# Performance work log

Measured on AMD Instinct MI355X. Metric: run time of the kernel, lower is better.

The kernel has to match this reference:

```python
import jax, jax.numpy as jnp
import numpy as np

N_NODES = 100000


def gcn_conv(x, edge_index, W, b, num_nodes):
    """PyG GCNConv: add self-loops, symmetric deg^{-1/2} normalization,
    aggregate (x @ W) over edges, then add bias."""
    loop = jnp.arange(num_nodes, dtype=edge_index.dtype)
    src = jnp.concatenate([edge_index[0], loop])  # [E+N]
    dst = jnp.concatenate([edge_index[1], loop])
    deg = jax.ops.segment_sum(jnp.ones_like(dst, dtype=x.dtype), dst,
                              num_segments=num_nodes)  # in-degree incl. self-loop
    dinv = jnp.where(deg > 0, jax.lax.rsqrt(deg), 0.0)
    norm = dinv[src] * dinv[dst]  # [E+N]
    h = x @ W  # [N, F_out] -- transform BEFORE gather (small F_out)
    msg = h[src] * norm[:, None]  # [E+N, F_out]
    out = jax.ops.segment_sum(msg, dst, num_segments=num_nodes)
    return out + b


def setup_inputs() -> dict:
    key = jax.random.key(0)
    k1, k2, k3, k4 = jax.random.split(key, 4)
    N, E, F_in, F_hid, F_out = N_NODES, 3200000, 128, 16, 64
    x = jax.random.normal(k1, (N, F_in), dtype=jnp.float32)
    edge_index = jax.random.randint(k2, (2, E), 0, N, dtype=jnp.int64)
    # glorot-ish init for weights, zeros bias (PyG default: glorot W, zeros b)
    W1 = jax.random.normal(k3, (F_in, F_hid), dtype=jnp.float32) * (1.0 / np.sqrt(F_in))
    b1 = jnp.zeros((F_hid,), dtype=jnp.float32)
    W2 = jax.random.normal(k4, (F_hid, F_out), dtype=jnp.float32) * (1.0 / np.sqrt(F_hid))
    b2 = jnp.zeros((F_out,), dtype=jnp.float32)
    return {"x": x, "edge_index": edge_index, "W1": W1, "b1": b1, "W2": W2, "b2": b2}


def reference(x, edge_index, W1, b1, W2, b2):
    N = x.shape[0]
    h = gcn_conv(x, edge_index, W1, b1, N)
    h = jax.nn.relu(h)
    # F.dropout with training=False (inference) is identity
    h = gcn_conv(h, edge_index, W2, b2, N)
    return jax.nn.log_softmax(h, axis=1)
```

## Files before the change

kernel.cpp:

```cpp
#include <hip/hip_runtime.h>

#define FIN 128
#define FH  16
#define FO  64
#define GB  128
#define MAXNB 1024
#define CHUNK 16384

__device__ __forceinline__ unsigned pack_bf16x2(float a, float b) {
    unsigned ua = __float_as_uint(a), ub = __float_as_uint(b);
    ua = (ua + 0x7fffu + ((ua >> 16) & 1u)) >> 16;
    ub = (ub + 0x7fffu + ((ub >> 16) & 1u)) >> 16;
    return ua | (ub << 16);
}

__device__ __forceinline__ float2 unpack_bf16x2(unsigned u) {
    float2 r;
    r.x = __uint_as_float(u << 16);
    r.y = __uint_as_float(u & 0xffff0000u);
    return r;
}

__global__ __launch_bounds__(1024) void k_bscatter(const int* __restrict__ src,
                                                   const int* __restrict__ dst,
                                                   int* __restrict__ bfill,
                                                   int* __restrict__ bedge,
                                                   int E, int slab) {
    __shared__ int h[MAXNB];
    __shared__ int scanp[1024];
    __shared__ int stage[CHUNK];
    int t = threadIdx.x;
    int c0 = blockIdx.x * CHUNK;
    int c1 = min(c0 + CHUNK, E);

    h[t] = 0;
    __syncthreads();
    const int4* dst4 = (const int4*)dst;
    const int4* src4 = (const int4*)src;
    int i4b = c0 >> 2;
    int i4e = (c0 + ((c1 - c0) & ~3)) >> 2;
    for (int i = i4b + t; i < i4e; i += 1024) {
        int4 d = dst4[i];
        atomicAdd(&h[d.x >> 7], 1);
        atomicAdd(&h[d.y >> 7], 1);
        atomicAdd(&h[d.z >> 7], 1);
        atomicAdd(&h[d.w >> 7], 1);
    }
    for (int e = (i4e << 2) + t; e < c1; e += 1024)
        atomicAdd(&h[dst[e] >> 7], 1);
    __syncthreads();

    int a = h[t];
    scanp[t] = a;
    __syncthreads();
    for (int off = 1; off < 1024; off <<= 1) {
        int u = (t >= off) ? scanp[t - off] : 0;
        __syncthreads();
        scanp[t] += u;
        __syncthreads();
    }
    int lo = scanp[t] - a;

    int r = 0;
    if (a) r = atomicAdd(&bfill[t], a);
    int navail = slab - r; if (navail < 0) navail = 0;
    int hi = lo + min(a, navail);
    h[t] = lo;
    __syncthreads();

    for (int i = i4b + t; i < i4e; i += 1024) {
        int4 d = dst4[i];
        int4 s = src4[i];
        int p;
        p = atomicAdd(&h[d.x >> 7], 1); stage[p] = ((d.x & 127) << 17) | s.x;
        p = atomicAdd(&h[d.y >> 7], 1); stage[p] = ((d.y & 127) << 17) | s.y;
        p = atomicAdd(&h[d.z >> 7], 1); stage[p] = ((d.z & 127) << 17) | s.z;
        p = atomicAdd(&h[d.w >> 7], 1); stage[p] = ((d.w & 127) << 17) | s.w;
    }
    for (int e = (i4e << 2) + t; e < c1; e += 1024) {
        int d = dst[e];
        int p = atomicAdd(&h[d >> 7], 1);
        stage[p] = ((d & 127) << 17) | src[e];
    }
    __syncthreads();

    int db = t * slab + r - lo;
    int p = lo;
    for (; p < hi && ((db + p) & 3); ++p) bedge[db + p] = stage[p];
    for (; p + 3 < hi; p += 4) {
        int4 v;
        v.x = stage[p]; v.y = stage[p + 1]; v.z = stage[p + 2]; v.w = stage[p + 3];
        *(int4*)(bedge + db + p) = v;
    }
    for (; p < hi; ++p) bedge[db + p] = stage[p];
}

__global__ __launch_bounds__(256) void k_nsg(const int* __restrict__ bfill,
                                             const int* __restrict__ bedge,
                                             const float* __restrict__ x,
                                             const float* __restrict__ W1,
                                             int* __restrict__ sorted_src,
                                             int* __restrict__ counts,
                                             int* __restrict__ row_start,
                                             float* __restrict__ dinv,
                                             uint2* __restrict__ hs1u2,
                                             int N, int slab) {
    __shared__ int hist[GB];
    __shared__ int fill[GB];
    __shared__ float dinvL[GB];
    __shared__ float4 w4[FIN * FH / 4];
    int t = threadIdx.x, b = blockIdx.x;
    int base = b << 7;
    int nn = min(GB, N - base);
    if (nn <= 0) return;

    int ebeg = b * slab;
    int eend = ebeg + min(bfill[b], slab);
    if (t < GB) hist[t] = 0;
    __syncthreads();
    for (int e = ebeg + t; e < eend; e += 256)
        atomicAdd(&hist[bedge[e] >> 17], 1);
    __syncthreads();
    int c = (t < GB) ? hist[t] : 0;
    for (int off = 1; off < GB; off <<= 1) {
        int u = (t < GB && t >= off) ? hist[t - off] : 0;
        __syncthreads();
        if (t < GB) hist[t] += u;
        __syncthreads();
    }
    int excl = (t < GB) ? hist[t] - c : 0;
    if (t < nn) {
        counts[base + t] = c;
        row_start[base + t] = ebeg + excl;
        float dv = rsqrtf((float)(c + 1));
        dinv[base + t] = dv;
        dinvL[t] = dv;
        fill[t] = ebeg + excl;
    }
    __syncthreads();
    for (int e = ebeg + t; e < eend; e += 256) {
        int v = bedge[e];
        int p = atomicAdd(&fill[v >> 17], 1);
        sorted_src[p] = v & 0x1FFFF;
    }
    for (int i = t; i < FIN * FH / 4; i += 256) w4[i] = ((const float4*)W1)[i];
    __syncthreads();

    int fg = t & 3, rg = t >> 2;
    int r0l = rg * 2;
    if (r0l >= nn) return;
    int r1l = min(r0l + 1, nn - 1);
    int r0 = base + r0l, r1 = base + r1l;
    const float4* xa4 = (const float4*)(x + (long long)r0 * FIN);
    const float4* xb4 = (const float4*)(x + (long long)r1 * FIN);
    float4 a0 = make_float4(0.f, 0.f, 0.f, 0.f);
    float4 a1 = make_float4(0.f, 0.f, 0.f, 0.f);
#pragma unroll 2
    for (int k4 = 0; k4 < FIN / 4; ++k4) {
        float4 xa = xa4[k4];
        float4 xb = xb4[k4];
        const float4* wp = &w4[k4 * 16 + fg];
        float4 w0 = wp[0], w1 = wp[4], w2 = wp[8], w3 = wp[12];
        a0.x = fmaf(xa.x, w0.x, a0.x); a0.y = fmaf(xa.x, w0.y, a0.y);
        a0.z = fmaf(xa.x, w0.z, a0.z); a0.w = fmaf(xa.x, w0.w, a0.w);
        a0.x = fmaf(xa.y, w1.x, a0.x); a0.y = fmaf(xa.y, w1.y, a0.y);
        a0.z = fmaf(xa.y, w1.z, a0.z); a0.w = fmaf(xa.y, w1.w, a0.w);
        a0.x = fmaf(xa.z, w2.x, a0.x); a0.y = fmaf(xa.z, w2.y, a0.y);
        a0.z = fmaf(xa.z, w2.z, a0.z); a0.w = fmaf(xa.z, w2.w, a0.w);
        a0.x = fmaf(xa.w, w3.x, a0.x); a0.y = fmaf(xa.w, w3.y, a0.y);
        a0.z = fmaf(xa.w, w3.z, a0.z); a0.w = fmaf(xa.w, w3.w, a0.w);
        a1.x = fmaf(xb.x, w0.x, a1.x); a1.y = fmaf(xb.x, w0.y, a1.y);
        a1.z = fmaf(xb.x, w0.z, a1.z); a1.w = fmaf(xb.x, w0.w, a1.w);
        a1.x = fmaf(xb.y, w1.x, a1.x); a1.y = fmaf(xb.y, w1.y, a1.y);
        a1.z = fmaf(xb.y, w1.z, a1.z); a1.w = fmaf(xb.y, w1.w, a1.w);
        a1.x = fmaf(xb.z, w2.x, a1.x); a1.y = fmaf(xb.z, w2.y, a1.y);
        a1.z = fmaf(xb.z, w2.z, a1.z); a1.w = fmaf(xb.z, w2.w, a1.w);
        a1.x = fmaf(xb.w, w3.x, a1.x); a1.y = fmaf(xb.w, w3.y, a1.y);
        a1.z = fmaf(xb.w, w3.z, a1.z); a1.w = fmaf(xb.w, w3.w, a1.w);
    }
    float d0 = dinvL[r0l];
    uint2 o0;
    o0.x = pack_bf16x2(a0.x * d0, a0.y * d0);
    o0.y = pack_bf16x2(a0.z * d0, a0.w * d0);
    hs1u2[r0 * 4 + fg] = o0;
    if (r1l != r0l) {
        float d1 = dinvL[r1l];
        uint2 o1;
        o1.x = pack_bf16x2(a1.x * d1, a1.y * d1);
        o1.y = pack_bf16x2(a1.z * d1, a1.w * d1);
        hs1u2[r1 * 4 + fg] = o1;
    }
}

__global__ __launch_bounds__(256) void k_gather1(const int* __restrict__ rs,
                                                 const int* __restrict__ cnt,
                                                 const int* __restrict__ ss,
                                                 const unsigned* __restrict__ hs1u,
                                                 const float* __restrict__ dinv,
                                                 const float* __restrict__ b1,
                                                 unsigned* __restrict__ h1su, int n) {
    int t = threadIdx.x;
    int lane = t & 63;
    int l32 = lane & 31, g4 = l32 >> 3, f2 = l32 & 7;
    int node = blockIdx.x * 8 + ((t >> 6) << 1) + (lane >> 5);
    bool act = (node < n);
    int beg = 0, end = 0;
    unsigned uself = 0;
    float di = 0.0f;
    if (act) {
        beg = rs[node]; end = beg + cnt[node];
        uself = hs1u[node * 8 + f2];
        di = dinv[node];
    }
    float ax = 0.0f, ay = 0.0f;
    int e = beg + g4;
    for (; e + 28 < end; e += 32) {
        int s0 = ss[e],      s1 = ss[e + 4],  s2 = ss[e + 8],  s3 = ss[e + 12];
        int s4 = ss[e + 16], s5 = ss[e + 20], s6 = ss[e + 24], s7 = ss[e + 28];
        unsigned u0 = hs1u[s0 * 8 + f2], u1 = hs1u[s1 * 8 + f2];
        unsigned u2 = hs1u[s2 * 8 + f2], u3 = hs1u[s3 * 8 + f2];
        unsigned u4 = hs1u[s4 * 8 + f2], u5 = hs1u[s5 * 8 + f2];
        unsigned u6 = hs1u[s6 * 8 + f2], u7 = hs1u[s7 * 8 + f2];
        float2 p0 = unpack_bf16x2(u0), p1 = unpack_bf16x2(u1);
        float2 p2 = unpack_bf16x2(u2), p3 = unpack_bf16x2(u3);
        float2 p4 = unpack_bf16x2(u4), p5 = unpack_bf16x2(u5);
        float2 p6 = unpack_bf16x2(u6), p7 = unpack_bf16x2(u7);
        ax += ((p0.x + p1.x) + (p2.x + p3.x)) + ((p4.x + p5.x) + (p6.x + p7.x));
        ay += ((p0.y + p1.y) + (p2.y + p3.y)) + ((p4.y + p5.y) + (p6.y + p7.y));
    }
    for (; e + 4 < end; e += 8) {
        int s0 = ss[e], s1 = ss[e + 4];
        unsigned u0 = hs1u[s0 * 8 + f2], u1 = hs1u[s1 * 8 + f2];
        float2 p0 = unpack_bf16x2(u0), p1 = unpack_bf16x2(u1);
        ax += p0.x + p1.x; ay += p0.y + p1.y;
    }
    if (e < end) {
        float2 p = unpack_bf16x2(hs1u[ss[e] * 8 + f2]);
        ax += p.x; ay += p.y;
    }
    ax += __shfl_xor(ax, 8, 64);  ay += __shfl_xor(ay, 8, 64);
    ax += __shfl_xor(ax, 16, 64); ay += __shfl_xor(ay, 16, 64);
    if (act) {
        float2 s = unpack_bf16x2(uself);
        ax += s.x; ay += s.y;
        float2 bb = ((const float2*)b1)[f2];
        float v0 = fmaxf(fmaf(di, ax, bb.x), 0.0f) * di;
        float v1 = fmaxf(fmaf(di, ay, bb.y), 0.0f) * di;
        if (l32 < 8) h1su[node * 8 + f2] = pack_bf16x2(v0, v1);
    }
}

__global__ __launch_bounds__(256) void k_agg2f(const int* __restrict__ rs,
                                               const int* __restrict__ cnt,
                                               const int* __restrict__ ss,
                                               const unsigned* __restrict__ h1su,
                                               const float* __restrict__ dinv,
                                               const float* __restrict__ W2,
                                               const float* __restrict__ b2,
                                               float* __restrict__ out, int n) {
    int t = threadIdx.x;
    int lane = t & 63, g8 = lane >> 3, f2 = lane & 7;
    int node = blockIdx.x * 4 + (t >> 6);
    if (node >= n) return;
    float w[FH];
#pragma unroll
    for (int j = 0; j < FH; ++j) w[j] = W2[j * FO + lane];
    int beg = rs[node], end = beg + cnt[node];
    float ax = 0.0f, ay = 0.0f;
    int e = beg + g8;
    for (; e + 8 < end; e += 16) {
        unsigned u0 = h1su[ss[e] * 8 + f2];
        unsigned u1 = h1su[ss[e + 8] * 8 + f2];
        float2 p0 = unpack_bf16x2(u0);
        float2 p1 = unpack_bf16x2(u1);
        ax += p0.x + p1.x; ay += p0.y + p1.y;
    }
    if (e < end) {
        float2 p = unpack_bf16x2(h1su[ss[e] * 8 + f2]);
        ax += p.x; ay += p.y;
    }
#pragma unroll
    for (int off = 8; off <= 32; off <<= 1) {
        ax += __shfl_xor(ax, off, 64);
        ay += __shfl_xor(ay, off, 64);
    }
    float2 s = unpack_bf16x2(h1su[node * 8 + f2]);
    ax += s.x; ay += s.y;
    float o = 0.0f;
#pragma unroll
    for (int j = 0; j < 8; ++j) {
        o = fmaf(__shfl(ax, j, 8), w[2 * j], o);
        o = fmaf(__shfl(ay, j, 8), w[2 * j + 1], o);
    }
    float v = fmaf(dinv[node], o, b2[lane]);
    float m = v;
#pragma unroll
    for (int off = 32; off >= 1; off >>= 1) m = fmaxf(m, __shfl_xor(m, off, 64));
    float ex = __expf(v - m);
#pragma unroll
    for (int off = 32; off >= 1; off >>= 1) ex += __shfl_xor(ex, off, 64);
    out[node * FO + lane] = v - m - __logf(ex);
}

extern "C" void kernel_launch(void* const* d_in, const int* in_sizes, int n_in,
                              void* d_out, int out_size, void* d_ws, size_t ws_size,
                              hipStream_t stream) {
    const float* x  = (const float*)d_in[0];
    const int*   ei = (const int*)d_in[1];
    const float* W1 = (const float*)d_in[2];
    const float* b1 = (const float*)d_in[3];
    const float* W2 = (const float*)d_in[4];
    const float* b2 = (const float*)d_in[5];
    float* out = (float*)d_out;

    int N = in_sizes[0] / FIN;
    int E = in_sizes[1] / 2;
    const int* src = ei;
    const int* dst = ei + E;
    int nb = (N + GB - 1) / GB;

    int slab = (E + nb - 1) / nb;
    slab = slab + slab / 4 + 1024;
    slab = (slab + 15) & ~15;
    long long slabtot = (long long)nb * slab;

    unsigned* hs1u  = (unsigned*)d_ws;
    unsigned* h1su  = hs1u + 8LL * N;
    int* bfill      = (int*)(h1su + 8LL * N);
    int* counts     = bfill + MAXNB;
    int* row_start  = counts + N;
    int* sorted_src = row_start + N;
    int* bedge      = sorted_src + slabtot;
    float* dinv     = (float*)(bedge + slabtot);

    hipMemsetAsync(bfill, 0, MAXNB * sizeof(int), stream);
    k_bscatter<<<(E + CHUNK - 1) / CHUNK, 1024, 0, stream>>>(src, dst, bfill, bedge, E, slab);
    k_nsg<<<nb, 256, 0, stream>>>(bfill, bedge, x, W1, sorted_src, counts, row_start,
                                  dinv, (uint2*)hs1u, N, slab);
    k_gather1<<<(N + 7) / 8, 256, 0, stream>>>(row_start, counts, sorted_src, hs1u, dinv, b1, h1su, N);
    k_agg2f<<<(N + 3) / 4, 256, 0, stream>>>(row_start, counts, sorted_src, h1su, dinv, W2, b2, out, N);
}
```

Baseline: 248.3 us.

## Process two nodes per wavefront in layer-2 aggregation with deeper load unrolling

The final aggregation kernel now maps two nodes to each 64-lane wavefront (32 lanes per node) instead of one, so the grid shrinks to N/8 blocks. The edge loop is unrolled eight-wide with index loads issued before the feature gathers, which raises memory-level parallelism, and a remainder loop handles the tail. Each lane computes two output features, and the softmax reductions run over 32 lanes. This cuts per-node lane waste and launch overhead, at the cost of more registers per thread and more divergence between the two nodes that share a wavefront.

```diff
diff --git a/kernel.cpp b/kernel.cpp
--- a/kernel.cpp
+++ b/kernel.cpp
@@ -259,47 +259,75 @@
                                                const float* __restrict__ b2,
                                                float* __restrict__ out, int n) {
     int t = threadIdx.x;
-    int lane = t & 63, g8 = lane >> 3, f2 = lane & 7;
-    int node = blockIdx.x * 4 + (t >> 6);
-    if (node >= n) return;
-    float w[FH];
-#pragma unroll
-    for (int j = 0; j < FH; ++j) w[j] = W2[j * FO + lane];
-    int beg = rs[node], end = beg + cnt[node];
+    int lane = t & 63;
+    int l32 = lane & 31, g4 = l32 >> 3, f2 = l32 & 7;
+    int node = blockIdx.x * 8 + ((t >> 6) << 1) + (lane >> 5);
+    bool act = (node < n);
+    int beg = 0, end = 0;
+    unsigned uself = 0;
+    float di = 0.0f;
+    if (act) {
+        beg = rs[node]; end = beg + cnt[node];
+        uself = h1su[node * 8 + f2];
+        di = dinv[node];
+    }
     float ax = 0.0f, ay = 0.0f;
-    int e = beg + g8;
-    for (; e + 8 < end; e += 16) {
-        unsigned u0 = h1su[ss[e] * 8 + f2];
-        unsigned u1 = h1su[ss[e + 8] * 8 + f2];
-        float2 p0 = unpack_bf16x2(u0);
-        float2 p1 = unpack_bf16x2(u1);
+    int e = beg + g4;
+    for (; e + 28 < end; e += 32) {
+        int s0 = ss[e],      s1 = ss[e + 4],  s2 = ss[e + 8],  s3 = ss[e + 12];
+        int s4 = ss[e + 16], s5 = ss[e + 20], s6 = ss[e + 24], s7 = ss[e + 28];
+        unsigned u0 = h1su[s0 * 8 + f2], u1 = h1su[s1 * 8 + f2];
+        unsigned u2 = h1su[s2 * 8 + f2], u3 = h1su[s3 * 8 + f2];
+        unsigned u4 = h1su[s4 * 8 + f2], u5 = h1su[s5 * 8 + f2];
+        unsigned u6 = h1su[s6 * 8 + f2], u7 = h1su[s7 * 8 + f2];
+        float2 p0 = unpack_bf16x2(u0), p1 = unpack_bf16x2(u1);
+        float2 p2 = unpack_bf16x2(u2), p3 = unpack_bf16x2(u3);
+        float2 p4 = unpack_bf16x2(u4), p5 = unpack_bf16x2(u5);
+        float2 p6 = unpack_bf16x2(u6), p7 = unpack_bf16x2(u7);
+        ax += ((p0.x + p1.x) + (p2.x + p3.x)) + ((p4.x + p5.x) + (p6.x + p7.x));
+        ay += ((p0.y + p1.y) + (p2.y + p3.y)) + ((p4.y + p5.y) + (p6.y + p7.y));
+    }
+    for (; e + 4 < end; e += 8) {
+        int s0 = ss[e], s1 = ss[e + 4];
+        unsigned u0 = h1su[s0 * 8 + f2], u1 = h1su[s1 * 8 + f2];
+        float2 p0 = unpack_bf16x2(u0), p1 = unpack_bf16x2(u1);
         ax += p0.x + p1.x; ay += p0.y + p1.y;
     }
     if (e < end) {
         float2 p = unpack_bf16x2(h1su[ss[e] * 8 + f2]);
         ax += p.x; ay += p.y;
     }
+    ax += __shfl_xor(ax, 8, 64);  ay += __shfl_xor(ay, 8, 64);
+    ax += __shfl_xor(ax, 16, 64); ay += __shfl_xor(ay, 16, 64);
+    float2 s = unpack_bf16x2(uself);
+    ax += s.x; ay += s.y;
+    float w0[FH], w1[FH];
 #pragma unroll
-    for (int off = 8; off <= 32; off <<= 1) {
-        ax += __shfl_xor(ax, off, 64);
-        ay += __shfl_xor(ay, off, 64);
-    }
-    float2 s = unpack_bf16x2(h1su[node * 8 + f2]);
-    ax += s.x; ay += s.y;
-    float o = 0.0f;
+    for (int j = 0; j < FH; ++j) {
+        w0[j] = W2[j * FO + l32];
+        w1[j] = W2[j * FO + l32 + 32];
+    }
+    float o0 = 0.0f, o1 = 0.0f;
 #pragma unroll
     for (int j = 0; j < 8; ++j) {
-        o = fmaf(__shfl(ax, j, 8), w[2 * j], o);
-        o = fmaf(__shfl(ay, j, 8), w[2 * j + 1], o);
-    }
-    float v = fmaf(dinv[node], o, b2[lane]);
-    float m = v;
+        float gx = __shfl(ax, j, 8), gy = __shfl(ay, j, 8);
+        o0 = fmaf(gx, w0[2 * j], o0); o0 = fmaf(gy, w0[2 * j + 1], o0);
+        o1 = fmaf(gx, w1[2 * j], o1); o1 = fmaf(gy, w1[2 * j + 1], o1);
+    }
+    float v0 = fmaf(di, o0, b2[l32]);
+    float v1 = fmaf(di, o1, b2[l32 + 32]);
+    float m = fmaxf(v0, v1);
 #pragma unroll
-    for (int off = 32; off >= 1; off >>= 1) m = fmaxf(m, __shfl_xor(m, off, 64));
-    float ex = __expf(v - m);
+    for (int off = 16; off >= 1; off >>= 1) m = fmaxf(m, __shfl_xor(m, off, 64));
+    float ex = __expf(v0 - m) + __expf(v1 - m);
 #pragma unroll
-    for (int off = 32; off >= 1; off >>= 1) ex += __shfl_xor(ex, off, 64);
-    out[node * FO + lane] = v - m - __logf(ex);
+    for (int off = 16; off >= 1; off >>= 1) ex += __shfl_xor(ex, off, 64);
+    float lse = m + __logf(ex);
+    if (act) {
+        float* orow = out + (long long)node * FO;
+        orow[l32]      = v0 - lse;
+        orow[l32 + 32] = v1 - lse;
+    }
 }
 
 extern "C" void kernel_launch(void* const* d_in, const int* in_sizes, int n_in,
@@ -338,5 +366,5 @@
     k_nsg<<<nb, 256, 0, stream>>>(bfill, bedge, x, W1, sorted_src, counts, row_start,
                                   dinv, (uint2*)hs1u, N, slab);
     k_gather1<<<(N + 7) / 8, 256, 0, stream>>>(row_start, counts, sorted_src, hs1u, dinv, b1, h1su, N);
-    k_agg2f<<<(N + 3) / 4, 256, 0, stream>>>(row_start, counts, sorted_src, h1su, dinv, W2, b2, out, N);
-}
+    k_agg2f<<<(N + 7) / 8, 256, 0, stream>>>(row_start, counts, sorted_src, h1su, dinv, W2, b2, out, N);
+}
```

Result: faster. 236.2 us (-4.9%).
